# Kernel tuning notes

Hardware: AMD Instinct MI355X
Metric: run time of the kernel (lower is better)

## Reference

```python
import jax, jax.numpy as jnp
import numpy as np

B, C_IN, C_OUT, N, K = 4, 64, 128, 81920, 10


def setup_inputs() -> dict:
    key = jax.random.key(0)
    k1, k2, k3, k4 = jax.random.split(key, 4)
    x = jax.random.normal(k1, (B, C_IN, N), dtype=jnp.float32)
    indices = jax.random.randint(k2, (N, K), 0, N, dtype=jnp.int64)
    # Conv2d(in, out, kernel=(1,K)) weight [C_out, C_in, 1, K] -> store as [C_out, C_in, K]
    fan_in = C_IN * K
    bound = 1.0 / np.sqrt(fan_in)
    W = jax.random.uniform(k3, (C_OUT, C_IN, K), jnp.float32, -bound, bound)
    b = jax.random.uniform(k4, (C_OUT,), jnp.float32, -bound, bound)
    return {"input": x, "indices": indices, "W": W, "b": b}


def reference(input, indices, W, b):
    # gather neighbor pixels: [B, C_in, N, K]
    col = input[:, :, indices]
    # 1xK conv == contraction over (C_in, K): [B, C_out, N]
    out = jnp.einsum('bcnk,ock->bon', col, W) + b[None, :, None]
    return out
```

## Files before the change

### kernel.cpp

```cpp
#include <hip/hip_runtime.h>
#include <hip/hip_bf16.h>
#include <stdint.h>

#define NPTS 81920
#define CIN  64
#define COUT 128
#define BATCH 4
#define KNB  10
#define NT   64

typedef __attribute__((ext_vector_type(8)))  short bf16x8;
typedef __attribute__((ext_vector_type(16))) float f32x16;

static __device__ __forceinline__ unsigned short f2bf(float f) {
    unsigned int u = __float_as_uint(f);
    u += 0x7fffu + ((u >> 16) & 1u);
    return (unsigned short)(u >> 16);
}

static __device__ __forceinline__ void gload16(const void* g, void* l) {
    __builtin_amdgcn_global_load_lds(
        (const __attribute__((address_space(1))) unsigned int*)g,
        (__attribute__((address_space(3))) unsigned int*)l, 16, 0, 0);
}

__global__ __launch_bounds__(256) void k_transpose(const float* __restrict__ x,
                                                   unsigned short* __restrict__ xT) {
    const int m = blockIdx.x * 256 + threadIdx.x;
    const int b = blockIdx.y;
    const float* xb = x + (size_t)b * CIN * NPTS + m;

    unsigned int v[CIN / 2];
    #pragma unroll
    for (int i = 0; i < CIN / 2; ++i) {
        float f0 = xb[(size_t)(2 * i) * NPTS];
        float f1 = xb[(size_t)(2 * i + 1) * NPTS];
        v[i] = (unsigned int)f2bf(f0) | ((unsigned int)f2bf(f1) << 16);
    }
    uint4* dst = (uint4*)(xT + ((size_t)m * BATCH + b) * CIN);
    #pragma unroll
    for (int i = 0; i < 8; ++i) {
        uint4 w; w.x = v[4*i]; w.y = v[4*i+1]; w.z = v[4*i+2]; w.w = v[4*i+3];
        dst[i] = w;
    }
}

__global__ __launch_bounds__(256) void k_wconv(const float* __restrict__ W,
                                               unsigned short* __restrict__ Wb) {
    const int e  = blockIdx.x * 256 + threadIdx.x;
    const int j  = e & 7;
    const int l  = (e >> 3) & 63;
    const int f  = (e >> 9) & 3;
    const int sg = e >> 11;
    const int o  = 32 * f + (l & 31);
    const int ck = sg * 16 + 8 * (l >> 5) + j;
    const int kn = ck >> 6;
    const int c  = ck & 63;
    Wb[e] = f2bf(W[(o * CIN + c) * KNB + kn]);
}

__global__ __launch_bounds__(256, 2) void k_main(const unsigned short* __restrict__ xT,
                                                 const unsigned short* __restrict__ Wb,
                                                 const float* __restrict__ bias,
                                                 const int* __restrict__ idx,
                                                 float* __restrict__ out) {
    __shared__ char smem[2][NT * 512];

    const int t    = threadIdx.x;
    const int lane = t & 63;
    const int wv   = t >> 6;
    const int ow2  = wv & 1;
    const int bq   = wv >> 1;
    const int hw   = lane >> 5;
    const int l31  = lane & 31;
    const int nb   = blockIdx.x * NT;

    const char* xb = (const char*)xT;
    const bf16x8* wbase = (const bf16x8*)Wb;

    f32x16 acc[2][2][2];
    #pragma unroll
    for (int p = 0; p < 2; ++p)
        #pragma unroll
        for (int nf = 0; nf < 2; ++nf)
            #pragma unroll
            for (int bb = 0; bb < 2; ++bb)
                #pragma unroll
                for (int r = 0; r < 16; ++r) acc[p][nf][bb][r] = 0.f;

    #define STAGE(kk, buf)                                                      \
        {                                                                       \
            _Pragma("unroll")                                                   \
            for (int i = 0; i < 8; ++i) {                                       \
                const int seg = (wv << 3) + i;                                  \
                const int row = (seg << 1) + (lane >> 5);                       \
                const int r   = idx[(nb + row) * KNB + (kk)];                   \
                const char* src = xb + (size_t)r * 512 +                        \
                                  ((((lane & 31) << 4)) ^ ((row & 7) << 4));    \
                gload16(src, &smem[buf][seg << 10]);                            \
            }                                                                   \
        }

    STAGE(0, 0);
    __syncthreads();

    #pragma unroll
    for (int k = 0; k < KNB; ++k) {
        if (k + 1 < KNB) STAGE(k + 1, (k + 1) & 1);

        bf16x8 a[2][4];
        #pragma unroll
        for (int p = 0; p < 2; ++p)
            #pragma unroll
            for (int ks = 0; ks < 4; ++ks)
                a[p][ks] = wbase[((k * 4 + ks) * 4 + (ow2 * 2 + p)) * 64 + lane];

        const char* sb = smem[k & 1];
        #pragma unroll
        for (int ks = 0; ks < 4; ++ks) {
            #pragma unroll
            for (int nf = 0; nf < 2; ++nf) {
                const int row = nf * 32 + l31;
                #pragma unroll
                for (int bb = 0; bb < 2; ++bb) {
                    const int b = bq * 2 + bb;
                    const int g = b * 8 + ks * 2 + hw;
                    const int byte = (g ^ (row & 7)) << 4;
                    const bf16x8 bf = *(const bf16x8*)(sb + row * 512 + byte);
                    #pragma unroll
                    for (int p = 0; p < 2; ++p)
                        acc[p][nf][bb] = __builtin_amdgcn_mfma_f32_32x32x16_bf16(
                            a[p][ks], bf, acc[p][nf][bb], 0, 0, 0);
                }
            }
        }
        __syncthreads();
    }
    #undef STAGE

    #pragma unroll
    for (int p = 0; p < 2; ++p) {
        #pragma unroll
        for (int nf = 0; nf < 2; ++nf) {
            const int n = nb + nf * 32 + l31;
            #pragma unroll
            for (int bb = 0; bb < 2; ++bb) {
                const int b = bq * 2 + bb;
                #pragma unroll
                for (int r = 0; r < 16; ++r) {
                    const int o = 32 * (ow2 * 2 + p) + (r & 3) + 8 * (r >> 2) + 4 * hw;
                    out[(size_t)(b * COUT + o) * NPTS + n] = acc[p][nf][bb][r] + bias[o];
                }
            }
        }
    }
}

extern "C" void kernel_launch(void* const* d_in, const int* in_sizes, int n_in,
                              void* d_out, int out_size, void* d_ws, size_t ws_size,
                              hipStream_t stream) {
    const float* x    = (const float*)d_in[0];
    const int*   idx  = (const int*)d_in[1];
    const float* W    = (const float*)d_in[2];
    const float* bias = (const float*)d_in[3];
    float* out = (float*)d_out;

    unsigned short* xT = (unsigned short*)d_ws;
    unsigned short* Wb = (unsigned short*)((char*)d_ws + (size_t)BATCH * NPTS * CIN * 2);

    k_transpose<<<dim3(NPTS / 256, BATCH), 256, 0, stream>>>(x, xT);
    k_wconv<<<dim3((COUT * KNB * CIN) / 256), 256, 0, stream>>>(W, Wb);
    k_main<<<dim3(NPTS / NT), 256, 0, stream>>>(xT, Wb, bias, idx, out);
}
```

Before: 159.5 us.

## Halve point tile, double waves per block, precompute gather offsets, nontemporal I/O

The main kernel moves from 64-point tiles with 4 waves to 32-point tiles with 8 waves per block. Each wave now owns one batch and a 64-channel output slice, holding 2 accumulators instead of 8. This cuts register pressure so launch bounds can ask for more resident waves to hide gather latency. Neighbor offsets for all 10 taps are loaded once up front instead of inside each stage, and the transpose loads and output stores use nontemporal hints. The cost is less weight-fragment reuse per wave (more redundant weight loads per MFMA) and twice as many blocks.

```diff
diff --git a/kernel.cpp b/kernel.cpp
--- a/kernel.cpp
+++ b/kernel.cpp
@@ -7,7 +7,7 @@
 #define COUT 128
 #define BATCH 4
 #define KNB  10
-#define NT   64
+#define NT   32
 
 typedef __attribute__((ext_vector_type(8)))  short bf16x8;
 typedef __attribute__((ext_vector_type(16))) float f32x16;
@@ -33,8 +33,8 @@
     unsigned int v[CIN / 2];
     #pragma unroll
     for (int i = 0; i < CIN / 2; ++i) {
-        float f0 = xb[(size_t)(2 * i) * NPTS];
-        float f1 = xb[(size_t)(2 * i + 1) * NPTS];
+        float f0 = __builtin_nontemporal_load(&xb[(size_t)(2 * i) * NPTS]);
+        float f1 = __builtin_nontemporal_load(&xb[(size_t)(2 * i + 1) * NPTS]);
         v[i] = (unsigned int)f2bf(f0) | ((unsigned int)f2bf(f1) << 16);
     }
     uint4* dst = (uint4*)(xT + ((size_t)m * BATCH + b) * CIN);
@@ -59,7 +59,7 @@
     Wb[e] = f2bf(W[(o * CIN + c) * KNB + kn]);
 }
 
-__global__ __launch_bounds__(256, 2) void k_main(const unsigned short* __restrict__ xT,
+__global__ __launch_bounds__(512, 4) void k_main(const unsigned short* __restrict__ xT,
                                                  const unsigned short* __restrict__ Wb,
                                                  const float* __restrict__ bias,
                                                  const int* __restrict__ idx,
@@ -69,8 +69,8 @@
     const int t    = threadIdx.x;
     const int lane = t & 63;
     const int wv   = t >> 6;
-    const int ow2  = wv & 1;
-    const int bq   = wv >> 1;
+    const int op   = wv & 1;
+    const int b    = wv >> 1;
     const int hw   = lane >> 5;
     const int l31  = lane & 31;
     const int nb   = blockIdx.x * NT;
@@ -78,26 +78,29 @@
     const char* xb = (const char*)xT;
     const bf16x8* wbase = (const bf16x8*)Wb;
 
-    f32x16 acc[2][2][2];
+    int soff[KNB][2];
+    #pragma unroll
+    for (int k = 0; k < KNB; ++k) {
+        #pragma unroll
+        for (int i = 0; i < 2; ++i) {
+            const int row = (wv << 2) + (i << 1) + hw;
+            const int r   = idx[(nb + row) * KNB + k];
+            soff[k][i] = r * 512 + ((l31 ^ (row & 7)) << 4);
+        }
+    }
+
+    f32x16 acc[2];
     #pragma unroll
     for (int p = 0; p < 2; ++p)
         #pragma unroll
-        for (int nf = 0; nf < 2; ++nf)
-            #pragma unroll
-            for (int bb = 0; bb < 2; ++bb)
-                #pragma unroll
-                for (int r = 0; r < 16; ++r) acc[p][nf][bb][r] = 0.f;
+        for (int r = 0; r < 16; ++r) acc[p][r] = 0.f;
 
     #define STAGE(kk, buf)                                                      \
         {                                                                       \
             _Pragma("unroll")                                                   \
-            for (int i = 0; i < 8; ++i) {                                       \
-                const int seg = (wv << 3) + i;                                  \
-                const int row = (seg << 1) + (lane >> 5);                       \
-                const int r   = idx[(nb + row) * KNB + (kk)];                   \
-                const char* src = xb + (size_t)r * 512 +                        \
-                                  ((((lane & 31) << 4)) ^ ((row & 7) << 4));    \
-                gload16(src, &smem[buf][seg << 10]);                            \
+            for (int i = 0; i < 2; ++i) {                                       \
+                gload16(xb + soff[kk][i],                                       \
+                        &smem[buf][(((wv << 2) + (i << 1))) << 9]);             \
             }                                                                   \
         }
 
@@ -113,45 +116,31 @@
         for (int p = 0; p < 2; ++p)
             #pragma unroll
             for (int ks = 0; ks < 4; ++ks)
-                a[p][ks] = wbase[((k * 4 + ks) * 4 + (ow2 * 2 + p)) * 64 + lane];
+                a[p][ks] = wbase[((k * 4 + ks) * 4 + (op * 2 + p)) * 64 + lane];
 
         const char* sb = smem[k & 1];
         #pragma unroll
         for (int ks = 0; ks < 4; ++ks) {
+            const int g    = b * 8 + ks * 2 + hw;
+            const int byte = (g ^ (l31 & 7)) << 4;
+            const bf16x8 bf = *(const bf16x8*)(sb + l31 * 512 + byte);
             #pragma unroll
-            for (int nf = 0; nf < 2; ++nf) {
-                const int row = nf * 32 + l31;
-                #pragma unroll
-                for (int bb = 0; bb < 2; ++bb) {
-                    const int b = bq * 2 + bb;
-                    const int g = b * 8 + ks * 2 + hw;
-                    const int byte = (g ^ (row & 7)) << 4;
-                    const bf16x8 bf = *(const bf16x8*)(sb + row * 512 + byte);
-                    #pragma unroll
-                    for (int p = 0; p < 2; ++p)
-                        acc[p][nf][bb] = __builtin_amdgcn_mfma_f32_32x32x16_bf16(
-                            a[p][ks], bf, acc[p][nf][bb], 0, 0, 0);
-                }
-            }
+            for (int p = 0; p < 2; ++p)
+                acc[p] = __builtin_amdgcn_mfma_f32_32x32x16_bf16(
+                    a[p][ks], bf, acc[p], 0, 0, 0);
         }
         __syncthreads();
     }
     #undef STAGE
 
+    const int n = nb + l31;
     #pragma unroll
     for (int p = 0; p < 2; ++p) {
         #pragma unroll
-        for (int nf = 0; nf < 2; ++nf) {
-            const int n = nb + nf * 32 + l31;
-            #pragma unroll
-            for (int bb = 0; bb < 2; ++bb) {
-                const int b = bq * 2 + bb;
-                #pragma unroll
-                for (int r = 0; r < 16; ++r) {
-                    const int o = 32 * (ow2 * 2 + p) + (r & 3) + 8 * (r >> 2) + 4 * hw;
-                    out[(size_t)(b * COUT + o) * NPTS + n] = acc[p][nf][bb][r] + bias[o];
-                }
-            }
+        for (int r = 0; r < 16; ++r) {
+            const int o = 32 * (op * 2 + p) + (r & 3) + 8 * (r >> 2) + 4 * hw;
+            const float v = acc[p][r] + bias[o];
+            __builtin_nontemporal_store(v, &out[(size_t)(b * COUT + o) * NPTS + n]);
         }
     }
 }
@@ -170,5 +159,5 @@
 
     k_transpose<<<dim3(NPTS / 256, BATCH), 256, 0, stream>>>(x, xT);
     k_wconv<<<dim3((COUT * KNB * CIN) / 256), 256, 0, stream>>>(W, Wb);
-    k_main<<<dim3(NPTS / NT), 256, 0, stream>>>(xT, Wb, bias, idx, out);
+    k_main<<<dim3(NPTS / NT), 512, 0, stream>>>(xT, Wb, bias, idx, out);
 }
```

Result: faster. 145.2 us (-9.0%).
